# Kernel optimization log

Measured on AMD Instinct MI355X. Metric: run time of the kernel, lower is better.

The kernel has to match this reference:

```python
import jax, jax.numpy as jnp
import numpy as np

N_NODES = 100000
N_EDGES = 3200000
N_GRAPHS = 1000
HID = 64
L = 4  # num_unit


def setup_inputs() -> dict:
    key = jax.random.key(0)
    ks = jax.random.split(key, 16)
    x = jax.random.normal(ks[0], (N_NODES, 4), dtype=jnp.float32)
    edge_index = jax.random.randint(ks[1], (2, N_EDGES), 0, N_NODES, dtype=jnp.int64)
    edge_attr = jax.random.uniform(ks[2], (N_EDGES,), dtype=jnp.float32)
    batch = jnp.sort(jax.random.randint(ks[3], (N_NODES,), 0, N_GRAPHS, dtype=jnp.int64))
    s = 1.0 / np.sqrt(HID)
    inp = {
        'x': x, 'edge_index': edge_index, 'edge_attr': edge_attr, 'batch': batch,
        'emb_w': jax.random.normal(ks[4], (4, HID), jnp.float32) * 0.5,
        'emb_b': jnp.zeros((HID,), jnp.float32),
        'conv_w1': jax.random.normal(ks[5], (L, HID, HID), jnp.float32) * s,
        'conv_b1': jnp.zeros((L, HID), jnp.float32),
        'conv_w2': jax.random.normal(ks[6], (L, HID, HID), jnp.float32) * s,
        'conv_w3': jax.random.normal(ks[7], (L, HID, HID), jnp.float32) * s,
        'conv_b3': jnp.zeros((L, HID), jnp.float32),
        'lin1_w': jax.random.normal(ks[8], (HID, HID), jnp.float32) * s,
        'lin1_b': jnp.zeros((HID,), jnp.float32),
        'lin2_w': jax.random.normal(ks[9], (HID, 3), jnp.float32) * s,
        'lin2_b': jnp.zeros((3,), jnp.float32),
    }
    return inp


def _forward(x, edge_index, edge_attr, batch,
             emb_w, emb_b, conv_w1, conv_b1, conv_w2, conv_w3, conv_b3,
             lin1_w, lin1_b, lin2_w, lin2_b):
    src, dst = edge_index[0], edge_index[1]
    ew = edge_attr[:, None]  # [E,1]
    h = x @ emb_w + emb_b  # node_emb; dropout omitted (eval mode)
    for l in range(conv_w1.shape[0]):
        # LEConv: out_i = sum_{j->i} w_ji * (lin1(x_j) - lin2(x_i)) + lin3(x_i)
        a = h @ conv_w1[l] + conv_b1[l]
        b = h @ conv_w2[l]  # no bias
        msg = (a[src] - b[dst]) * ew  # [E, HID]
        agg = jax.ops.segment_sum(msg, dst, num_segments=h.shape[0])
        h = jax.nn.relu(agg + h @ conv_w3[l] + conv_b3[l])
    # global mean pool over graphs
    sums = jax.ops.segment_sum(h, batch, num_segments=N_GRAPHS)
    cnt = jax.ops.segment_sum(jnp.ones((h.shape[0],), h.dtype), batch, num_segments=N_GRAPHS)
    graph_x = sums / jnp.maximum(cnt, 1.0)[:, None]
    pred = jax.nn.relu(graph_x @ lin1_w + lin1_b) @ lin2_w + lin2_b
    return pred


def reference(x, edge_index, edge_attr, batch, emb_w, emb_b,
              conv_w1, conv_b1, conv_w2, conv_w3, conv_b3,
              lin1_w, lin1_b, lin2_w, lin2_b):
    return _forward(x, edge_index, edge_attr, batch, emb_w, emb_b,
                    conv_w1, conv_b1, conv_w2, conv_w3, conv_b3,
                    lin1_w, lin1_b, lin2_w, lin2_b)
```

## Files before the change

kernel.cpp:

```cpp
#include <hip/hip_runtime.h>

#define N_NODES 100000
#define N_EDGES 3200000
#define N_GRAPHS 1000
#define NLAYER 4
#define NB 391
#define CAP 8960
#define EPB 4096
#define NCHUNK 782

typedef __attribute__((ext_vector_type(8))) short bf16x8;
typedef __attribute__((ext_vector_type(4))) float f32x4;

static __device__ __forceinline__ unsigned f2bf(float f) {
  unsigned u = __float_as_uint(f);
  return (u + 0x7fffu + ((u >> 16) & 1u)) >> 16;
}
static __device__ __forceinline__ float bf2f_lo(unsigned u) {
  return __uint_as_float(u << 16);
}
static __device__ __forceinline__ float bf2f_hi(unsigned u) {
  return __uint_as_float(u & 0xffff0000u);
}

__global__ __launch_bounds__(256) void prologue_kernel(
    const float* __restrict__ x, const float* __restrict__ emb_w,
    const float* __restrict__ emb_b, unsigned short* __restrict__ h_bf,
    int* __restrict__ gcur,
    const float* __restrict__ cw1, const float* __restrict__ cw2,
    const float* __restrict__ cw3, unsigned* __restrict__ wswz)
{
  int tid = threadIdx.x;
  if (blockIdx.x == 4) {
    for (int i = tid; i < NB; i += 256) gcur[i] = i * CAP;
  }
  if (blockIdx.x < NLAYER) {
    int l = blockIdx.x;
    const float* w1 = cw1 + l * 4096;
    const float* w2 = cw2 + l * 4096;
    const float* w3 = cw3 + l * 4096;
    unsigned* outp = wswz + l * 6144;
    int n = tid & 63;
    int gofs = tid >> 6;
    for (int it = 0; it < 24; ++it) {
      int g = it * 4 + gofs;
      int m = g >> 5;
      int k = (g & 31) * 2;
      const float* W = (m == 0) ? w2 : (m == 1) ? w3 : w1;
      unsigned lo = f2bf(W[k * 64 + n]);
      unsigned hi = f2bf(W[(k + 1) * 64 + n]);
      int c = k >> 5;
      int kk = k & 31;
      int ln = ((kk >> 3) << 4) | (n & 15);
      int j2 = (kk & 7) >> 1;
      int t4 = n >> 4;
      outp[(((m * 2 + c) * 4 + t4) << 8) | (ln << 2) | j2] = lo | (hi << 16);
    }
  }
  int t = blockIdx.x * 256 + tid;
  if (t >= N_NODES * 64) return;
  int c = t & 63, v = t >> 6;
  float4 xv = ((const float4*)x)[v];
  float acc = emb_b[c];
  acc = fmaf(xv.x, emb_w[0 * 64 + c], acc);
  acc = fmaf(xv.y, emb_w[1 * 64 + c], acc);
  acc = fmaf(xv.z, emb_w[2 * 64 + c], acc);
  acc = fmaf(xv.w, emb_w[3 * 64 + c], acc);
  h_bf[t] = (unsigned short)f2bf(acc);
}

__global__ __launch_bounds__(256) void bscatter_kernel(
    const int* __restrict__ ei, const float* __restrict__ ea,
    int* __restrict__ gcur, unsigned* __restrict__ tmp_w,
    unsigned char* __restrict__ tmp_d)
{
  __shared__ unsigned hist[NB];
  __shared__ int dif[NB];
  __shared__ unsigned stage_w[EPB];
  __shared__ unsigned char stage_d[EPB];
  __shared__ unsigned short bid[EPB];
  __shared__ int wpart[4];
  int tid = threadIdx.x;
  int base = blockIdx.x * EPB;

  for (int i = tid; i < NB; i += 256) hist[i] = 0;
  __syncthreads();

  int dreg[16];
#pragma unroll
  for (int i = 0; i < 16; ++i) {
    int e = base + i * 256 + tid;
    dreg[i] = -1;
    if (e < N_EDGES) {
      int d = ei[N_EDGES + e];
      dreg[i] = d;
      atomicAdd(&hist[((unsigned)d) >> 8], 1u);
    }
  }
  __syncthreads();

  int lane = tid & 63, w = tid >> 6;
  int b0i = tid * 2, b1i = tid * 2 + 1;
  int c0 = (b0i < NB) ? (int)hist[b0i] : 0;
  int c1 = (b1i < NB) ? (int)hist[b1i] : 0;
  int tsum = c0 + c1;
  int s = tsum;
#pragma unroll
  for (int off = 1; off < 64; off <<= 1) {
    int y = __shfl_up(s, off);
    if (lane >= off) s += y;
  }
  if (lane == 63) wpart[w] = s;
  __syncthreads();
  int wo = 0;
  for (int ww = 0; ww < w; ++ww) wo += wpart[ww];
  int excl = wo + (s - tsum);
  if (b0i < NB) {
    int gb = c0 ? atomicAdd(&gcur[b0i], c0) : 0;
    dif[b0i] = gb - excl;
    hist[b0i] = (unsigned)excl;
  }
  if (b1i < NB) {
    int gb = c1 ? atomicAdd(&gcur[b1i], c1) : 0;
    dif[b1i] = gb - (excl + c0);
    hist[b1i] = (unsigned)(excl + c0);
  }
  __syncthreads();

#pragma unroll
  for (int i = 0; i < 16; ++i) {
    int e = base + i * 256 + tid;
    int d = dreg[i];
    if (d >= 0) {
      unsigned bkt = ((unsigned)d) >> 8;
      unsigned lp = atomicAdd(&hist[bkt], 1u);
      unsigned q15 = (unsigned)(ea[e] * 32768.0f);
      stage_w[lp] = ((unsigned)ei[e]) | (q15 << 17);
      stage_d[lp] = (unsigned char)(d & 255);
      bid[lp] = (unsigned short)bkt;
    }
  }
  __syncthreads();

  int nE = min(EPB, N_EDGES - base);
  for (int i = tid; i < nE; i += 256) {
    int g = dif[bid[i]] + i;
    tmp_w[g] = stage_w[i];
    tmp_d[g] = stage_d[i];
  }
}

__global__ __launch_bounds__(256) void bucket_sort_kernel(
    const int* __restrict__ gcur, const unsigned* __restrict__ tmp_w,
    const unsigned char* __restrict__ tmp_d,
    unsigned* __restrict__ csr, int* __restrict__ row_off,
    unsigned short* __restrict__ deg16, float* __restrict__ degw)
{
  int j = blockIdx.x;
  int b0 = j * CAP;
  int nE = min(gcur[j] - b0, CAP);
  __shared__ unsigned hist[256];
  __shared__ float dws[256];
  __shared__ unsigned cur[256];
  __shared__ int wpart[4];
  __shared__ unsigned short perm[CAP];
  int t = threadIdx.x;
  hist[t] = 0;
  dws[t] = 0.f;
  __syncthreads();
  for (int i = t; i < nE; i += 256) {
    unsigned d = tmp_d[b0 + i];
    unsigned wrd = tmp_w[b0 + i];
    atomicAdd(&hist[d], 1u);
    atomicAdd(&dws[d], (float)(wrd >> 17) * (1.0f / 32768.0f));
  }
  __syncthreads();
  int lane = t & 63, w = t >> 6;
  int v = (int)hist[t];
  int s = v;
#pragma unroll
  for (int off = 1; off < 64; off <<= 1) {
    int y = __shfl_up(s, off);
    if (lane >= off) s += y;
  }
  if (lane == 63) wpart[w] = s;
  __syncthreads();
  int wo = 0;
  for (int ww = 0; ww < w; ++ww) wo += wpart[ww];
  int excl = wo + s - v;
  cur[t] = (unsigned)excl;
  int vnode = (j << 8) + t;
  if (vnode < N_NODES) {
    row_off[vnode] = b0 + excl;
    deg16[vnode] = (unsigned short)v;
    degw[vnode] = dws[t];
  }
  __syncthreads();

  for (int i = t; i < nE; i += 256) {
    unsigned p = atomicAdd(&cur[tmp_d[b0 + i]], 1u);
    perm[p] = (unsigned short)i;
  }
  __syncthreads();
  for (int q = t; q < nE; q += 256)
    csr[b0 + q] = tmp_w[b0 + (int)perm[q]];
}

__global__ __launch_bounds__(256) void matvec3_mfma_kernel(
    const unsigned short* __restrict__ h_bf,
    const unsigned* __restrict__ wz,
    const float* __restrict__ b1, const float* __restrict__ b3,
    const float* __restrict__ degw,
    unsigned short* __restrict__ a_bf, unsigned short* __restrict__ cc_bf)
{
  int gw = (blockIdx.x * 256 + threadIdx.x) >> 6;
  int lane = threadIdx.x & 63;
  int quad = lane >> 4;
  int col = lane & 15;
  int nb = gw * 16;
  if (nb >= N_NODES) return;

  int arow = nb + col;
  if (arow >= N_NODES) arow = N_NODES - 1;
  const bf16x8* ap = (const bf16x8*)(h_bf + (size_t)arow * 64 + quad * 8);
  bf16x8 af0 = ap[0];
  bf16x8 af1 = ap[4];

  float dwr[4];
#pragma unroll
  for (int r = 0; r < 4; ++r) {
    int row = nb + quad * 4 + r;
    dwr[r] = degw[row < N_NODES ? row : 0];
  }

#pragma unroll
  for (int t = 0; t < 4; ++t) {
    const bf16x8* b20 = (const bf16x8*)&wz[((0 * 4 + t) << 8) + lane * 4];
    const bf16x8* b21 = (const bf16x8*)&wz[((1 * 4 + t) << 8) + lane * 4];
    const bf16x8* b30 = (const bf16x8*)&wz[((2 * 4 + t) << 8) + lane * 4];
    const bf16x8* b31 = (const bf16x8*)&wz[((3 * 4 + t) << 8) + lane * 4];
    const bf16x8* b10 = (const bf16x8*)&wz[((4 * 4 + t) << 8) + lane * 4];
    const bf16x8* b11 = (const bf16x8*)&wz[((5 * 4 + t) << 8) + lane * 4];

    f32x4 z = {0.f, 0.f, 0.f, 0.f};
    f32x4 acc2 = __builtin_amdgcn_mfma_f32_16x16x32_bf16(af0, *b20, z, 0, 0, 0);
    acc2 = __builtin_amdgcn_mfma_f32_16x16x32_bf16(af1, *b21, acc2, 0, 0, 0);
    f32x4 cc;
#pragma unroll
    for (int r = 0; r < 4; ++r) cc[r] = -dwr[r] * acc2[r];
    cc = __builtin_amdgcn_mfma_f32_16x16x32_bf16(af0, *b30, cc, 0, 0, 0);
    cc = __builtin_amdgcn_mfma_f32_16x16x32_bf16(af1, *b31, cc, 0, 0, 0);
    float bb3 = b3[t * 16 + col];
#pragma unroll
    for (int r = 0; r < 4; ++r) {
      int row = nb + quad * 4 + r;
      if (row < N_NODES)
        cc_bf[(size_t)row * 64 + t * 16 + col] = (unsigned short)f2bf(cc[r] + bb3);
    }

    float bb1 = b1[t * 16 + col];
    f32x4 a1 = {bb1, bb1, bb1, bb1};
    a1 = __builtin_amdgcn_mfma_f32_16x16x32_bf16(af0, *b10, a1, 0, 0, 0);
    a1 = __builtin_amdgcn_mfma_f32_16x16x32_bf16(af1, *b11, a1, 0, 0, 0);
#pragma unroll
    for (int r = 0; r < 4; ++r) {
      int row = nb + quad * 4 + r;
      if (row < N_NODES)
        a_bf[(size_t)row * 64 + t * 16 + col] = (unsigned short)f2bf(a1[r]);
    }
  }
}

__global__ __launch_bounds__(256) void agg_kernel(
    const uint2* __restrict__ a2, const uint2* __restrict__ cc2,
    const int* __restrict__ row_off, const unsigned short* __restrict__ deg16,
    const unsigned* __restrict__ csr,
    float4* __restrict__ h4, unsigned short* __restrict__ h_bf, int write_h)
{
  int wave = (blockIdx.x * 256 + threadIdx.x) >> 6;
  int lane = threadIdx.x & 63;
  int sg = lane >> 4;
  int li = lane & 15;
  int lsel = (lane & 48) << 2;
  int v = wave * 4 + sg;
  bool valid = v < N_NODES;
  int vc = valid ? v : N_NODES - 1;
  int base = row_off[vc];
  int ecnt = valid ? (int)deg16[vc] : 0;
  int emax = ecnt;
  emax = max(emax, __shfl_xor(emax, 16));
  emax = max(emax, __shfl_xor(emax, 32));

  float4 acc = make_float4(0.f, 0.f, 0.f, 0.f);
  if (valid) {
    uint2 cu = cc2[(size_t)vc * 16 + li];
    acc.x = bf2f_lo(cu.x);
    acc.y = bf2f_hi(cu.x);
    acc.z = bf2f_lo(cu.y);
    acc.w = bf2f_hi(cu.y);
  }
  const uint2* ap = a2 + li;

  int full = emax & ~15;
  int c0 = 0;
  for (; c0 < full; c0 += 16) {
    int idx = c0 + li;
    int er = (idx < ecnt) ? (int)csr[base + idx] : 0;
#pragma unroll
    for (int j = 0; j < 16; ++j) {
      unsigned r = (unsigned)__builtin_amdgcn_ds_bpermute(lsel | (j << 2), er);
      int s = (int)(r & 0x1FFFFu);
      float w = (float)(r >> 17) * (1.0f / 32768.0f);
      uint2 u = ap[(size_t)s * 16];
      acc.x = fmaf(w, bf2f_lo(u.x), acc.x);
      acc.y = fmaf(w, bf2f_hi(u.x), acc.y);
      acc.z = fmaf(w, bf2f_lo(u.y), acc.z);
      acc.w = fmaf(w, bf2f_hi(u.y), acc.w);
    }
  }
  int rem = emax - full;
  if (rem > 0) {
    int idx = c0 + li;
    int er = (idx < ecnt) ? (int)csr[base + idx] : 0;
    for (int j = 0; j < rem; ++j) {
      unsigned r = (unsigned)__builtin_amdgcn_ds_bpermute(lsel | (j << 2), er);
      int s = (int)(r & 0x1FFFFu);
      float w = (float)(r >> 17) * (1.0f / 32768.0f);
      uint2 u = ap[(size_t)s * 16];
      acc.x = fmaf(w, bf2f_lo(u.x), acc.x);
      acc.y = fmaf(w, bf2f_hi(u.x), acc.y);
      acc.z = fmaf(w, bf2f_lo(u.y), acc.z);
      acc.w = fmaf(w, bf2f_hi(u.y), acc.w);
    }
  }
  if (valid) {
    acc.x = fmaxf(acc.x, 0.f);
    acc.y = fmaxf(acc.y, 0.f);
    acc.z = fmaxf(acc.z, 0.f);
    acc.w = fmaxf(acc.w, 0.f);
    if (write_h) h4[(size_t)v * 16 + li] = acc;
    uint2 p;
    p.x = f2bf(acc.x) | (f2bf(acc.y) << 16);
    p.y = f2bf(acc.z) | (f2bf(acc.w) << 16);
    ((uint2*)h_bf)[(size_t)v * 16 + li] = p;
  }
}

__global__ __launch_bounds__(256) void head_kernel(
    const float* __restrict__ h, const int* __restrict__ batch,
    const float* __restrict__ l1w, const float* __restrict__ l1b,
    const float* __restrict__ l2w, const float* __restrict__ l2b,
    float* __restrict__ out)
{
  int g = (blockIdx.x * 256 + threadIdx.x) >> 6;
  int lane = threadIdx.x & 63;
  if (g >= N_GRAPHS) return;
  int lo = 0, hi = N_NODES;
  while (lo < hi) { int mid = (lo + hi) >> 1; if (batch[mid] < g) lo = mid + 1; else hi = mid; }
  int start = lo;
  hi = N_NODES;
  while (lo < hi) { int mid = (lo + hi) >> 1; if (batch[mid] < g + 1) lo = mid + 1; else hi = mid; }
  int end = lo;

  float sum = 0.f;
  for (int v = start; v < end; ++v) sum += h[(size_t)v * 64 + lane];
  float cntf = (float)(end - start);
  float gx = sum / fmaxf(cntf, 1.f);

  float acc = l1b[lane];
  for (int k = 0; k < 64; ++k) {
    float gxk = __shfl(gx, k);
    acc = fmaf(gxk, l1w[k * 64 + lane], acc);
  }
  float t = fmaxf(acc, 0.f);
  float p0 = t * l2w[lane * 3 + 0];
  float p1 = t * l2w[lane * 3 + 1];
  float p2 = t * l2w[lane * 3 + 2];
  for (int off = 32; off > 0; off >>= 1) {
    p0 += __shfl_down(p0, off);
    p1 += __shfl_down(p1, off);
    p2 += __shfl_down(p2, off);
  }
  if (lane == 0) {
    out[g * 3 + 0] = p0 + l2b[0];
    out[g * 3 + 1] = p1 + l2b[1];
    out[g * 3 + 2] = p2 + l2b[2];
  }
}

extern "C" void kernel_launch(void* const* d_in, const int* in_sizes, int n_in,
                              void* d_out, int out_size, void* d_ws, size_t ws_size,
                              hipStream_t stream)
{
  (void)in_sizes; (void)n_in; (void)out_size; (void)ws_size;
  const float* x     = (const float*)d_in[0];
  const int*   ei    = (const int*)d_in[1];
  const float* ea    = (const float*)d_in[2];
  const int*   batch = (const int*)d_in[3];
  const float* emb_w = (const float*)d_in[4];
  const float* emb_b = (const float*)d_in[5];
  const float* cw1   = (const float*)d_in[6];
  const float* cb1   = (const float*)d_in[7];
  const float* cw2   = (const float*)d_in[8];
  const float* cw3   = (const float*)d_in[9];
  const float* cb3   = (const float*)d_in[10];
  const float* l1w   = (const float*)d_in[11];
  const float* l1b   = (const float*)d_in[12];
  const float* l2w   = (const float*)d_in[13];
  const float* l2b   = (const float*)d_in[14];
  float* out = (float*)d_out;

  char* wsb = (char*)d_ws;
  size_t off = 0;
  auto alloc = [&](size_t bytes) {
    char* p = wsb + off;
    off = (off + bytes + 255) & ~(size_t)255;
    return p;
  };
  float* h       = (float*)alloc(sizeof(float) * (size_t)N_NODES * 64);
  unsigned short* h_bf = (unsigned short*)alloc(sizeof(short) * (size_t)N_NODES * 64);
  unsigned short* a_bf = (unsigned short*)alloc(sizeof(short) * (size_t)N_NODES * 64);
  unsigned short* cc_bf = (unsigned short*)alloc(sizeof(short) * (size_t)N_NODES * 64);
  unsigned* csr  = (unsigned*)alloc(sizeof(unsigned) * (size_t)NB * CAP);
  int*   row_off = (int*)alloc(sizeof(int) * N_NODES);
  unsigned short* deg16 = (unsigned short*)alloc(sizeof(short) * N_NODES);
  float* degw    = (float*)alloc(sizeof(float) * N_NODES);
  int*   gcur    = (int*)alloc(sizeof(int) * NB);
  unsigned* wswz = (unsigned*)alloc(sizeof(unsigned) * NLAYER * 6144);
  unsigned* tmp_w = (unsigned*)h;
  unsigned char* tmp_d = (unsigned char*)h + sizeof(unsigned) * (size_t)NB * CAP;

  prologue_kernel<<<(N_NODES * 64 + 255) / 256, 256, 0, stream>>>(
      x, emb_w, emb_b, h_bf, gcur, cw1, cw2, cw3, wswz);
  bscatter_kernel<<<NCHUNK, 256, 0, stream>>>(ei, ea, gcur, tmp_w, tmp_d);
  bucket_sort_kernel<<<NB, 256, 0, stream>>>(gcur, tmp_w, tmp_d, csr, row_off,
                                             deg16, degw);

  int agg_blocks = (N_NODES + 15) / 16;
  int mv_blocks = (N_NODES / 16 + 3) / 4 + 1;
  for (int l = 0; l < NLAYER; ++l) {
    matvec3_mfma_kernel<<<mv_blocks, 256, 0, stream>>>(
        h_bf, wswz + l * 6144, cb1 + l * 64, cb3 + l * 64, degw, a_bf, cc_bf);
    agg_kernel<<<agg_blocks, 256, 0, stream>>>(
        (const uint2*)a_bf, (const uint2*)cc_bf, row_off, deg16, csr, (float4*)h,
        h_bf, (l == NLAYER - 1) ? 1 : 0);
  }

  head_kernel<<<(N_GRAPHS * 64 + 255) / 256, 256, 0, stream>>>(
      h, batch, l1w, l1b, l2w, l2b, out);
}
```

Measured before the change: 520.2 us.

## Split gather table into feature halves and aggregate each half separately

The per-layer 'a' table is split into two 32-feature halves stored in separate arrays. The aggregation kernel walks each node's edge list twice, gathering one half per pass, so each pass touches a 6.4MB table that fits better in cache, at the cost of re-reading the CSR and redoing the index shuffles. The fp32 h output is dropped and the head kernel pools from the bf16 h instead, which loses some precision. The edge scatter also reads source index and weight in the first pass and keeps them in registers, and the temporary buffers get their own workspace allocation.

Measured after the change: 644.2 us. +23.8%, slower.

```diff
diff --git a/kernel.cpp b/kernel.cpp
--- a/kernel.cpp
+++ b/kernel.cpp
@@ -87,6 +87,7 @@
   __syncthreads();
 
   int dreg[16];
+  unsigned wreg[16];
 #pragma unroll
   for (int i = 0; i < 16; ++i) {
     int e = base + i * 256 + tid;
@@ -94,6 +95,8 @@
     if (e < N_EDGES) {
       int d = ei[N_EDGES + e];
       dreg[i] = d;
+      unsigned q15 = (unsigned)(ea[e] * 32768.0f);
+      wreg[i] = ((unsigned)ei[e]) | (q15 << 17);
       atomicAdd(&hist[((unsigned)d) >> 8], 1u);
     }
   }
@@ -129,13 +132,11 @@
 
 #pragma unroll
   for (int i = 0; i < 16; ++i) {
-    int e = base + i * 256 + tid;
     int d = dreg[i];
     if (d >= 0) {
       unsigned bkt = ((unsigned)d) >> 8;
       unsigned lp = atomicAdd(&hist[bkt], 1u);
-      unsigned q15 = (unsigned)(ea[e] * 32768.0f);
-      stage_w[lp] = ((unsigned)ei[e]) | (q15 << 17);
+      stage_w[lp] = wreg[i];
       stage_d[lp] = (unsigned char)(d & 255);
       bid[lp] = (unsigned short)bkt;
     }
@@ -211,7 +212,8 @@
     const unsigned* __restrict__ wz,
     const float* __restrict__ b1, const float* __restrict__ b3,
     const float* __restrict__ degw,
-    unsigned short* __restrict__ a_bf, unsigned short* __restrict__ cc_bf)
+    unsigned short* __restrict__ a_lo, unsigned short* __restrict__ a_hi,
+    unsigned short* __restrict__ cc_bf)
 {
   int gw = (blockIdx.x * 256 + threadIdx.x) >> 6;
   int lane = threadIdx.x & 63;
@@ -265,17 +267,22 @@
 #pragma unroll
     for (int r = 0; r < 4; ++r) {
       int row = nb + quad * 4 + r;
-      if (row < N_NODES)
-        a_bf[(size_t)row * 64 + t * 16 + col] = (unsigned short)f2bf(a1[r]);
+      if (row < N_NODES) {
+        if (t < 2)
+          a_lo[(size_t)row * 32 + t * 16 + col] = (unsigned short)f2bf(a1[r]);
+        else
+          a_hi[(size_t)row * 32 + (t - 2) * 16 + col] = (unsigned short)f2bf(a1[r]);
+      }
     }
   }
 }
 
 __global__ __launch_bounds__(256) void agg_kernel(
-    const uint2* __restrict__ a2, const uint2* __restrict__ cc2,
+    const unsigned* __restrict__ alo, const unsigned* __restrict__ ahi,
+    const unsigned* __restrict__ ccw,
     const int* __restrict__ row_off, const unsigned short* __restrict__ deg16,
     const unsigned* __restrict__ csr,
-    float4* __restrict__ h4, unsigned short* __restrict__ h_bf, int write_h)
+    unsigned short* __restrict__ h_bf)
 {
   int wave = (blockIdx.x * 256 + threadIdx.x) >> 6;
   int lane = threadIdx.x & 63;
@@ -290,64 +297,53 @@
   int emax = ecnt;
   emax = max(emax, __shfl_xor(emax, 16));
   emax = max(emax, __shfl_xor(emax, 32));
-
-  float4 acc = make_float4(0.f, 0.f, 0.f, 0.f);
-  if (valid) {
-    uint2 cu = cc2[(size_t)vc * 16 + li];
-    acc.x = bf2f_lo(cu.x);
-    acc.y = bf2f_hi(cu.x);
-    acc.z = bf2f_lo(cu.y);
-    acc.w = bf2f_hi(cu.y);
-  }
-  const uint2* ap = a2 + li;
-
   int full = emax & ~15;
-  int c0 = 0;
-  for (; c0 < full; c0 += 16) {
-    int idx = c0 + li;
-    int er = (idx < ecnt) ? (int)csr[base + idx] : 0;
-#pragma unroll
-    for (int j = 0; j < 16; ++j) {
-      unsigned r = (unsigned)__builtin_amdgcn_ds_bpermute(lsel | (j << 2), er);
-      int s = (int)(r & 0x1FFFFu);
-      float w = (float)(r >> 17) * (1.0f / 32768.0f);
-      uint2 u = ap[(size_t)s * 16];
-      acc.x = fmaf(w, bf2f_lo(u.x), acc.x);
-      acc.y = fmaf(w, bf2f_hi(u.x), acc.y);
-      acc.z = fmaf(w, bf2f_lo(u.y), acc.z);
-      acc.w = fmaf(w, bf2f_hi(u.y), acc.w);
-    }
-  }
-  int rem = emax - full;
-  if (rem > 0) {
-    int idx = c0 + li;
-    int er = (idx < ecnt) ? (int)csr[base + idx] : 0;
-    for (int j = 0; j < rem; ++j) {
-      unsigned r = (unsigned)__builtin_amdgcn_ds_bpermute(lsel | (j << 2), er);
-      int s = (int)(r & 0x1FFFFu);
-      float w = (float)(r >> 17) * (1.0f / 32768.0f);
-      uint2 u = ap[(size_t)s * 16];
-      acc.x = fmaf(w, bf2f_lo(u.x), acc.x);
-      acc.y = fmaf(w, bf2f_hi(u.x), acc.y);
-      acc.z = fmaf(w, bf2f_lo(u.y), acc.z);
-      acc.w = fmaf(w, bf2f_hi(u.y), acc.w);
-    }
-  }
-  if (valid) {
-    acc.x = fmaxf(acc.x, 0.f);
-    acc.y = fmaxf(acc.y, 0.f);
-    acc.z = fmaxf(acc.z, 0.f);
-    acc.w = fmaxf(acc.w, 0.f);
-    if (write_h) h4[(size_t)v * 16 + li] = acc;
-    uint2 p;
-    p.x = f2bf(acc.x) | (f2bf(acc.y) << 16);
-    p.y = f2bf(acc.z) | (f2bf(acc.w) << 16);
-    ((uint2*)h_bf)[(size_t)v * 16 + li] = p;
+
+#pragma unroll 1
+  for (int hf = 0; hf < 2; ++hf) {
+    const unsigned* ah = hf ? ahi : alo;
+    unsigned cu = ccw[(size_t)vc * 32 + hf * 16 + li];
+    float ax = bf2f_lo(cu);
+    float ay = bf2f_hi(cu);
+
+    int c0 = 0;
+    for (; c0 < full; c0 += 16) {
+      int idx = c0 + li;
+      int er = (idx < ecnt) ? (int)csr[base + idx] : 0;
+#pragma unroll
+      for (int j = 0; j < 16; ++j) {
+        unsigned r = (unsigned)__builtin_amdgcn_ds_bpermute(lsel | (j << 2), er);
+        int s = (int)(r & 0x1FFFFu);
+        float w = (float)(r >> 17) * (1.0f / 32768.0f);
+        unsigned u = ah[(size_t)s * 16 + li];
+        ax = fmaf(w, bf2f_lo(u), ax);
+        ay = fmaf(w, bf2f_hi(u), ay);
+      }
+    }
+    int rem = emax - full;
+    if (rem > 0) {
+      int idx = c0 + li;
+      int er = (idx < ecnt) ? (int)csr[base + idx] : 0;
+      for (int j = 0; j < rem; ++j) {
+        unsigned r = (unsigned)__builtin_amdgcn_ds_bpermute(lsel | (j << 2), er);
+        int s = (int)(r & 0x1FFFFu);
+        float w = (float)(r >> 17) * (1.0f / 32768.0f);
+        unsigned u = ah[(size_t)s * 16 + li];
+        ax = fmaf(w, bf2f_lo(u), ax);
+        ay = fmaf(w, bf2f_hi(u), ay);
+      }
+    }
+    if (valid) {
+      ax = fmaxf(ax, 0.f);
+      ay = fmaxf(ay, 0.f);
+      ((unsigned*)h_bf)[(size_t)v * 32 + hf * 16 + li] =
+          f2bf(ax) | (f2bf(ay) << 16);
+    }
   }
 }
 
 __global__ __launch_bounds__(256) void head_kernel(
-    const float* __restrict__ h, const int* __restrict__ batch,
+    const unsigned short* __restrict__ h_bf, const int* __restrict__ batch,
     const float* __restrict__ l1w, const float* __restrict__ l1b,
     const float* __restrict__ l2w, const float* __restrict__ l2b,
     float* __restrict__ out)
@@ -363,7 +359,8 @@
   int end = lo;
 
   float sum = 0.f;
-  for (int v = start; v < end; ++v) sum += h[(size_t)v * 64 + lane];
+  for (int v = start; v < end; ++v)
+    sum += bf2f_lo((unsigned)h_bf[(size_t)v * 64 + lane]);
   float cntf = (float)(end - start);
   float gx = sum / fmaxf(cntf, 1.f);
 
@@ -417,18 +414,18 @@
     off = (off + bytes + 255) & ~(size_t)255;
     return p;
   };
-  float* h       = (float*)alloc(sizeof(float) * (size_t)N_NODES * 64);
   unsigned short* h_bf = (unsigned short*)alloc(sizeof(short) * (size_t)N_NODES * 64);
-  unsigned short* a_bf = (unsigned short*)alloc(sizeof(short) * (size_t)N_NODES * 64);
+  unsigned short* a_lo = (unsigned short*)alloc(sizeof(short) * (size_t)N_NODES * 32);
+  unsigned short* a_hi = (unsigned short*)alloc(sizeof(short) * (size_t)N_NODES * 32);
   unsigned short* cc_bf = (unsigned short*)alloc(sizeof(short) * (size_t)N_NODES * 64);
   unsigned* csr  = (unsigned*)alloc(sizeof(unsigned) * (size_t)NB * CAP);
+  unsigned* tmp_w = (unsigned*)alloc(sizeof(unsigned) * (size_t)NB * CAP);
+  unsigned char* tmp_d = (unsigned char*)alloc((size_t)NB * CAP);
   int*   row_off = (int*)alloc(sizeof(int) * N_NODES);
   unsigned short* deg16 = (unsigned short*)alloc(sizeof(short) * N_NODES);
   float* degw    = (float*)alloc(sizeof(float) * N_NODES);
   int*   gcur    = (int*)alloc(sizeof(int) * NB);
   unsigned* wswz = (unsigned*)alloc(sizeof(unsigned) * NLAYER * 6144);
-  unsigned* tmp_w = (unsigned*)h;
-  unsigned char* tmp_d = (unsigned char*)h + sizeof(unsigned) * (size_t)NB * CAP;
 
   prologue_kernel<<<(N_NODES * 64 + 255) / 256, 256, 0, stream>>>(
       x, emb_w, emb_b, h_bf, gcur, cw1, cw2, cw3, wswz);
@@ -440,12 +437,13 @@
   int mv_blocks = (N_NODES / 16 + 3) / 4 + 1;
   for (int l = 0; l < NLAYER; ++l) {
     matvec3_mfma_kernel<<<mv_blocks, 256, 0, stream>>>(
-        h_bf, wswz + l * 6144, cb1 + l * 64, cb3 + l * 64, degw, a_bf, cc_bf);
+        h_bf, wswz + l * 6144, cb1 + l * 64, cb3 + l * 64, degw, a_lo, a_hi,
+        cc_bf);
     agg_kernel<<<agg_blocks, 256, 0, stream>>>(
-        (const uint2*)a_bf, (const uint2*)cc_bf, row_off, deg16, csr, (float4*)h,
-        h_bf, (l == NLAYER - 1) ? 1 : 0);
+        (const unsigned*)a_lo, (const unsigned*)a_hi, (const unsigned*)cc_bf,
+        row_off, deg16, csr, h_bf);
   }
 
   head_kernel<<<(N_GRAPHS * 64 + 255) / 256, 256, 0, stream>>>(
-      h, batch, l1w, l1b, l2w, l2b, out);
-}
+      h_bf, batch, l1w, l1b, l2w, l2b, out);
+}
```
